# Kernel optimization log

Measured on AMD Instinct MI355X. Metric: run time of the kernel, lower is better.

Reference implementation:

```python
import jax, jax.numpy as jnp
import numpy as np

B, N, D = 256, 50, 128
NEG = -9e15  # torch uses -9000000000000000.0
LEAKY_SLOPE = 0.2


def setup_inputs() -> dict:
    key = jax.random.key(0)
    ks = jax.random.split(key, 6)
    hidden = jax.random.normal(ks[0], (B, N, D), dtype=jnp.float32)
    adj = jax.random.randint(ks[1], (B, N, N), 0, 5)  # edge types 0..4
    a_0 = jax.random.normal(ks[2], (D, 1), dtype=jnp.float32) * 0.05
    a_1 = jax.random.normal(ks[3], (D, 1), dtype=jnp.float32) * 0.05
    a_2 = jax.random.normal(ks[4], (D, 1), dtype=jnp.float32) * 0.05
    a_3 = jax.random.normal(ks[5], (D, 1), dtype=jnp.float32) * 0.05
    return {"hidden": hidden, "adj": adj, "a_0": a_0, "a_1": a_1, "a_2": a_2, "a_3": a_3}


def reference(hidden, adj, a_0, a_1, a_2, a_3):
    # LocalAggregator.forward (typed-edge GAT over session graph).
    # Original builds a_input[b,i,j,:] = h[b,i,:]*h[b,j,:] (B,N,N,D) then
    # projects with 4 relation vectors a_k (D,1). We fuse: stack the 4
    # vectors and contract D in one einsum -> e[b,k,i,j].
    A = jnp.concatenate([a_0, a_1, a_2, a_3], axis=1)          # (D, 4)
    e = jnp.einsum('bid,bjd,dk->bkij', hidden, hidden, A)      # (B, 4, N, N)
    e = jax.nn.leaky_relu(e, negative_slope=LEAKY_SLOPE)
    # Per-edge-type masking: adj value v in {1..4} selects branch v-1,
    # anything else gets -9e15 (same chained torch.where semantics/order).
    scores = jnp.full_like(e[:, 0], NEG)                        # (B, N, N)
    scores = jnp.where(adj == 1, e[:, 0], scores)
    scores = jnp.where(adj == 2, e[:, 1], scores)
    scores = jnp.where(adj == 3, e[:, 2], scores)
    scores = jnp.where(adj == 4, e[:, 3], scores)
    attn = jax.nn.softmax(scores, axis=-1)                      # (B, N, N)
    return jnp.einsum('bij,bjd->bid', attn, hidden)             # (B, N, D)
```

## Files before the change

kernel.cpp:

```cpp
#include <hip/hip_runtime.h>
#include <stdint.h>

typedef __attribute__((ext_vector_type(8))) short short8;
typedef __attribute__((ext_vector_type(4))) float f32x4;

namespace {
constexpr int   kN     = 50;
constexpr int   kD     = 128;
constexpr float kNeg   = -9.0e15f;
constexpr float kSlope = 0.2f;
constexpr int   HS32   = 132;
constexpr int   HS16   = 136;
constexpr int   ADS    = 52;
constexpr int   PS     = 20;
}

union Pack8 { uint32_t u[4]; short8 s; };

__global__ __launch_bounds__(512)
void gat_v11_kernel(const float* __restrict__ hidden,
                    const int*   __restrict__ adj,
                    const float* __restrict__ a0,
                    const float* __restrict__ a1,
                    const float* __restrict__ a2,
                    const float* __restrict__ a3,
                    float* __restrict__ out)
{
    __shared__ float          Hf [kN * HS32];
    __shared__ unsigned short Hhi[64 * HS16];
    __shared__ unsigned short Hlo[64 * HS16];
    __shared__ unsigned char  Ad [kN * ADS];
    __shared__ float          Xch[8][64][16];
    __shared__ unsigned short Pw [8][64 * PS];

    const int b    = blockIdx.x;
    const int tid  = threadIdx.x;
    const int lane = tid & 63;
    const int wid  = __builtin_amdgcn_readfirstlane(tid >> 6);
    const int g    = lane >> 4;
    const int f    = lane & 15;

    const float* __restrict__ hb   = hidden + (size_t)b * (kN * kD);
    const int*   __restrict__ adjb = adj    + (size_t)b * (kN * kN);
    float*       __restrict__ outb = out    + (size_t)b * (kN * kD);

    const float4* hg = reinterpret_cast<const float4*>(hb);
    #pragma unroll
    for (int it4 = 0; it4 < 4; ++it4) {
        const int idx = tid + it4 * 512;
        const int j   = idx >> 5;
        const int d4  = idx & 31;
        float4 v = make_float4(0.f, 0.f, 0.f, 0.f);
        if (j < kN) v = hg[j * 32 + d4];

        const uint32_t h0 = __float_as_uint(v.x) & 0xffff0000u;
        const uint32_t h1 = __float_as_uint(v.y) & 0xffff0000u;
        const uint32_t h2 = __float_as_uint(v.z) & 0xffff0000u;
        const uint32_t h3 = __float_as_uint(v.w) & 0xffff0000u;
        uint2 hiw;
        hiw.x = h1 | (h0 >> 16);
        hiw.y = h3 | (h2 >> 16);
        const float r0 = v.x - __uint_as_float(h0);
        const float r1 = v.y - __uint_as_float(h1);
        const float r2 = v.z - __uint_as_float(h2);
        const float r3 = v.w - __uint_as_float(h3);
        uint2 low;
        low.x = (__float_as_uint(r1) & 0xffff0000u) | (__float_as_uint(r0) >> 16);
        low.y = (__float_as_uint(r3) & 0xffff0000u) | (__float_as_uint(r2) >> 16);
        *reinterpret_cast<uint2*>(&Hhi[j * HS16 + 4 * d4]) = hiw;
        *reinterpret_cast<uint2*>(&Hlo[j * HS16 + 4 * d4]) = low;
        if (j < kN) *reinterpret_cast<float4*>(&Hf[j * HS32 + 4 * d4]) = v;
    }
    for (int idx = tid; idx < 625; idx += 512) {
        const int4 v = reinterpret_cast<const int4*>(adjb)[idx];
        const int e = 4 * idx;
        const int vv[4] = {v.x, v.y, v.z, v.w};
        #pragma unroll
        for (int p = 0; p < 4; ++p) {
            const int ee  = e + p;
            const int row = ee / kN;
            const int col = ee - kN * row;
            Ad[row * ADS + col] = (unsigned char)vv[p];
        }
    }
    __syncthreads();

    const int it   = wid & 3;
    const int kh   = wid >> 2;
    const int i0   = 16 * it;
    const int irow = (i0 + f < kN) ? (i0 + f) : (kN - 1);

    f32x4 acc[4][4];
    #pragma unroll
    for (int jt = 0; jt < 4; ++jt)
        #pragma unroll
        for (int k = 0; k < 4; ++k) acc[jt][k] = (f32x4){0.f, 0.f, 0.f, 0.f};

    const float* __restrict__ aks[4] = {a0, a1, a2, a3};

    #pragma unroll
    for (int ksl2 = 0; ksl2 < 2; ++ksl2) {
        const int dofs = 64 * kh + 32 * ksl2 + 8 * g;

        const float4 hA0 = *reinterpret_cast<const float4*>(&Hf[irow * HS32 + dofs]);
        const float4 hA1 = *reinterpret_cast<const float4*>(&Hf[irow * HS32 + dofs + 4]);
        const float ha[8] = {hA0.x, hA0.y, hA0.z, hA0.w, hA1.x, hA1.y, hA1.z, hA1.w};

        short8 qh[4], ql[4];
        #pragma unroll
        for (int k = 0; k < 4; ++k) {
            const float4 av0 = *reinterpret_cast<const float4*>(aks[k] + dofs);
            const float4 av1 = *reinterpret_cast<const float4*>(aks[k] + dofs + 4);
            const float aa[8] = {av0.x, av0.y, av0.z, av0.w, av1.x, av1.y, av1.z, av1.w};
            Pack8 ph, pl;
            #pragma unroll
            for (int p = 0; p < 4; ++p) {
                const float q0 = ha[2 * p]     * aa[2 * p];
                const float q1 = ha[2 * p + 1] * aa[2 * p + 1];
                const uint32_t b0 = __float_as_uint(q0) & 0xffff0000u;
                const uint32_t b1 = __float_as_uint(q1) & 0xffff0000u;
                ph.u[p] = b1 | (b0 >> 16);
                const float s0 = q0 - __uint_as_float(b0);
                const float s1 = q1 - __uint_as_float(b1);
                pl.u[p] = (__float_as_uint(s1) & 0xffff0000u) | (__float_as_uint(s0) >> 16);
            }
            qh[k] = ph.s;
            ql[k] = pl.s;
        }

        #pragma unroll
        for (int jt = 0; jt < 4; ++jt) {
            const int jrow = 16 * jt + f;
            const short8 bh = *reinterpret_cast<const short8*>(&Hhi[jrow * HS16 + dofs]);
            const short8 bl = *reinterpret_cast<const short8*>(&Hlo[jrow * HS16 + dofs]);
            #pragma unroll
            for (int k = 0; k < 4; ++k) {
                acc[jt][k] = __builtin_amdgcn_mfma_f32_16x16x32_bf16(qh[k], bh, acc[jt][k], 0, 0, 0);
                acc[jt][k] = __builtin_amdgcn_mfma_f32_16x16x32_bf16(qh[k], bl, acc[jt][k], 0, 0, 0);
                acc[jt][k] = __builtin_amdgcn_mfma_f32_16x16x32_bf16(ql[k], bh, acc[jt][k], 0, 0, 0);
            }
        }
    }

    f32x4 spart[4];
    uint32_t vmask = 0;
    #pragma unroll
    for (int jt = 0; jt < 4; ++jt) {
        const int j = 16 * jt + f;
        #pragma unroll
        for (int reg = 0; reg < 4; ++reg) {
            const int ii  = i0 + 4 * g + reg;
            const int iic = (ii < kN) ? ii : (kN - 1);
            int kv = 0;
            if (j < kN) kv = Ad[iic * ADS + j];
            const bool valid = (kv >= 1) && (kv <= 4);
            spart[jt][reg] = (kv == 1) ? acc[jt][0][reg]
                           : (kv == 2) ? acc[jt][1][reg]
                           : (kv == 3) ? acc[jt][2][reg]
                           : (kv == 4) ? acc[jt][3][reg] : 0.f;
            vmask |= (valid ? 1u : 0u) << (4 * jt + reg);
        }
    }

    #pragma unroll
    for (int jt = 0; jt < 4; ++jt)
        *reinterpret_cast<f32x4*>(&Xch[wid][lane][4 * jt]) = spart[jt];
    __syncthreads();

    float s[4][4];
    #pragma unroll
    for (int jt = 0; jt < 4; ++jt) {
        const f32x4 o = *reinterpret_cast<const f32x4*>(&Xch[wid ^ 4][lane][4 * jt]);
        #pragma unroll
        for (int reg = 0; reg < 4; ++reg) {
            const float x  = spart[jt][reg] + o[reg];
            const float lx = (x > 0.f) ? x : kSlope * x;
            s[jt][reg] = ((vmask >> (4 * jt + reg)) & 1u) ? lx : kNeg;
        }
    }

    #pragma unroll
    for (int reg = 0; reg < 4; ++reg) {
        float m = fmaxf(fmaxf(s[0][reg], s[1][reg]), fmaxf(s[2][reg], s[3][reg]));
        #pragma unroll
        for (int o = 1; o < 16; o <<= 1) m = fmaxf(m, __shfl_xor(m, o));

        float e[4];
        float t = 0.f;
        #pragma unroll
        for (int jt = 0; jt < 4; ++jt) {
            const int j = 16 * jt + f;
            e[jt] = (j < kN) ? __expf(s[jt][reg] - m) : 0.f;
            t += e[jt];
        }
        #pragma unroll
        for (int o = 1; o < 16; o <<= 1) t += __shfl_xor(t, o);

        const float inv = 1.0f / t;
        #pragma unroll
        for (int jt = 0; jt < 4; ++jt) {
            uint32_t u = __float_as_uint(e[jt] * inv);
            u += 0x7fffu + ((u >> 16) & 1u);
            Pw[wid][(16 * jt + f) * PS + 4 * g + reg] = (unsigned short)(u >> 16);
        }
    }

    {
        const int db = 64 * kh + 4 * f;
        f32x4 o0 = {0.f, 0.f, 0.f, 0.f}, o1 = o0, o2 = o0, o3 = o0;
        #pragma unroll 5
        for (int j = 0; j < kN; ++j) {
            const float4  hv = *reinterpret_cast<const float4*>(&Hf[j * HS32 + db]);
            const ushort4 p4 = *reinterpret_cast<const ushort4*>(&Pw[wid][j * PS + 4 * g]);
            const float av0 = __uint_as_float(((uint32_t)p4.x) << 16);
            const float av1 = __uint_as_float(((uint32_t)p4.y) << 16);
            const float av2 = __uint_as_float(((uint32_t)p4.z) << 16);
            const float av3 = __uint_as_float(((uint32_t)p4.w) << 16);
            o0.x += av0 * hv.x; o0.y += av0 * hv.y; o0.z += av0 * hv.z; o0.w += av0 * hv.w;
            o1.x += av1 * hv.x; o1.y += av1 * hv.y; o1.z += av1 * hv.z; o1.w += av1 * hv.w;
            o2.x += av2 * hv.x; o2.y += av2 * hv.y; o2.z += av2 * hv.z; o2.w += av2 * hv.w;
            o3.x += av3 * hv.x; o3.y += av3 * hv.y; o3.z += av3 * hv.z; o3.w += av3 * hv.w;
        }
        const int rbase = i0 + 4 * g;
        if (rbase + 0 < kN) *reinterpret_cast<f32x4*>(&outb[(rbase + 0) * kD + db]) = o0;
        if (rbase + 1 < kN) *reinterpret_cast<f32x4*>(&outb[(rbase + 1) * kD + db]) = o1;
        if (rbase + 2 < kN) *reinterpret_cast<f32x4*>(&outb[(rbase + 2) * kD + db]) = o2;
        if (rbase + 3 < kN) *reinterpret_cast<f32x4*>(&outb[(rbase + 3) * kD + db]) = o3;
    }
}

extern "C" void kernel_launch(void* const* d_in, const int* in_sizes, int n_in,
                              void* d_out, int out_size, void* d_ws, size_t ws_size,
                              hipStream_t stream) {
    const float* hidden = reinterpret_cast<const float*>(d_in[0]);
    const int*   adjp   = reinterpret_cast<const int*>(d_in[1]);
    const float* a0     = reinterpret_cast<const float*>(d_in[2]);
    const float* a1     = reinterpret_cast<const float*>(d_in[3]);
    const float* a2     = reinterpret_cast<const float*>(d_in[4]);
    const float* a3     = reinterpret_cast<const float*>(d_in[5]);
    float*       outp   = reinterpret_cast<float*>(d_out);

    gat_v11_kernel<<<dim3(256), dim3(512), 0, stream>>>(
        hidden, adjp, a0, a1, a2, a3, outp);
}
```

Baseline: 17.76 us.

## Compute attention-times-hidden with bf16 hi/lo MFMA using transposed split hidden

Replaces the scalar FMA loop for attn @ hidden with MFMA 16x16x32 bf16 instructions. Hidden is stored in a transposed, packed hi/lo bf16 layout so that two MFMAs (hi and lo parts) keep near-fp32 accuracy on the hidden operand. The fp32 hidden copy in shared memory is dropped, and the query row is rebuilt from the hi/lo halves. The price is an extra transposed staging pass at load time with strided LDS writes, plus unpacking work before each MFMA. Output stores become scalar rather than float4.

```diff
diff --git a/kernel.cpp b/kernel.cpp
--- a/kernel.cpp
+++ b/kernel.cpp
@@ -9,16 +9,23 @@
 constexpr int   kD     = 128;
 constexpr float kNeg   = -9.0e15f;
 constexpr float kSlope = 0.2f;
-constexpr int   HS32   = 132;
 constexpr int   HS16   = 136;
 constexpr int   ADS    = 52;
-constexpr int   PS     = 20;
+constexpr int   HTW    = 66;
+constexpr int   PW     = 72;
 }
 
 union Pack8 { uint32_t u[4]; short8 s; };
 
+__device__ __forceinline__ uint32_t pack_hl(float v) {
+    const uint32_t b  = __float_as_uint(v);
+    const uint32_t hi = b & 0xffff0000u;
+    const float    r  = v - __uint_as_float(hi);
+    return (b >> 16) | (__float_as_uint(r) & 0xffff0000u);
+}
+
 __global__ __launch_bounds__(512)
-void gat_v11_kernel(const float* __restrict__ hidden,
+void gat_v12_kernel(const float* __restrict__ hidden,
                     const int*   __restrict__ adj,
                     const float* __restrict__ a0,
                     const float* __restrict__ a1,
@@ -26,12 +33,12 @@
                     const float* __restrict__ a3,
                     float* __restrict__ out)
 {
-    __shared__ float          Hf [kN * HS32];
     __shared__ unsigned short Hhi[64 * HS16];
     __shared__ unsigned short Hlo[64 * HS16];
+    __shared__ uint32_t       Hti[128 * HTW];
     __shared__ unsigned char  Ad [kN * ADS];
     __shared__ float          Xch[8][64][16];
-    __shared__ unsigned short Pw [8][64 * PS];
+    __shared__ unsigned short Pw2[8][16 * PW];
 
     const int b    = blockIdx.x;
     const int tid  = threadIdx.x;
@@ -69,7 +76,6 @@
         low.y = (__float_as_uint(r3) & 0xffff0000u) | (__float_as_uint(r2) >> 16);
         *reinterpret_cast<uint2*>(&Hhi[j * HS16 + 4 * d4]) = hiw;
         *reinterpret_cast<uint2*>(&Hlo[j * HS16 + 4 * d4]) = low;
-        if (j < kN) *reinterpret_cast<float4*>(&Hf[j * HS32 + 4 * d4]) = v;
     }
     for (int idx = tid; idx < 625; idx += 512) {
         const int4 v = reinterpret_cast<const int4*>(adjb)[idx];
@@ -83,6 +89,21 @@
             Ad[row * ADS + col] = (unsigned char)vv[p];
         }
     }
+    const float2* hb2 = reinterpret_cast<const float2*>(hb);
+    #pragma unroll
+    for (int it4 = 0; it4 < 4; ++it4) {
+        const int jp = wid + 8 * it4;
+        const int j0 = 2 * jp, j1 = 2 * jp + 1;
+        const int d2 = lane;
+        float2 v0 = make_float2(0.f, 0.f), v1 = v0;
+        if (j0 < kN) v0 = hb2[j0 * 64 + d2];
+        if (j1 < kN) v1 = hb2[j1 * 64 + d2];
+        uint2 wa, wb;
+        wa.x = pack_hl(v0.x); wa.y = pack_hl(v1.x);
+        wb.x = pack_hl(v0.y); wb.y = pack_hl(v1.y);
+        *reinterpret_cast<uint2*>(&Hti[(2 * d2 + 0) * HTW + j0]) = wa;
+        *reinterpret_cast<uint2*>(&Hti[(2 * d2 + 1) * HTW + j0]) = wb;
+    }
     __syncthreads();
 
     const int it   = wid & 3;
@@ -102,9 +123,15 @@
     for (int ksl2 = 0; ksl2 < 2; ++ksl2) {
         const int dofs = 64 * kh + 32 * ksl2 + 8 * g;
 
-        const float4 hA0 = *reinterpret_cast<const float4*>(&Hf[irow * HS32 + dofs]);
-        const float4 hA1 = *reinterpret_cast<const float4*>(&Hf[irow * HS32 + dofs + 4]);
-        const float ha[8] = {hA0.x, hA0.y, hA0.z, hA0.w, hA1.x, hA1.y, hA1.z, hA1.w};
+        const short8 ah8 = *reinterpret_cast<const short8*>(&Hhi[irow * HS16 + dofs]);
+        const short8 al8 = *reinterpret_cast<const short8*>(&Hlo[irow * HS16 + dofs]);
+        float ha[8];
+        #pragma unroll
+        for (int p = 0; p < 8; ++p) {
+            const uint32_t uh = ((uint32_t)(unsigned short)ah8[p]) << 16;
+            const uint32_t ul = ((uint32_t)(unsigned short)al8[p]) << 16;
+            ha[p] = __uint_as_float(uh) + __uint_as_float(ul);
+        }
 
         short8 qh[4], ql[4];
         #pragma unroll
@@ -201,31 +228,54 @@
         for (int jt = 0; jt < 4; ++jt) {
             uint32_t u = __float_as_uint(e[jt] * inv);
             u += 0x7fffu + ((u >> 16) & 1u);
-            Pw[wid][(16 * jt + f) * PS + 4 * g + reg] = (unsigned short)(u >> 16);
+            Pw2[wid][(4 * g + reg) * PW + 16 * jt + f] = (unsigned short)(u >> 16);
         }
     }
 
     {
-        const int db = 64 * kh + 4 * f;
-        f32x4 o0 = {0.f, 0.f, 0.f, 0.f}, o1 = o0, o2 = o0, o3 = o0;
-        #pragma unroll 5
-        for (int j = 0; j < kN; ++j) {
-            const float4  hv = *reinterpret_cast<const float4*>(&Hf[j * HS32 + db]);
-            const ushort4 p4 = *reinterpret_cast<const ushort4*>(&Pw[wid][j * PS + 4 * g]);
-            const float av0 = __uint_as_float(((uint32_t)p4.x) << 16);
-            const float av1 = __uint_as_float(((uint32_t)p4.y) << 16);
-            const float av2 = __uint_as_float(((uint32_t)p4.z) << 16);
-            const float av3 = __uint_as_float(((uint32_t)p4.w) << 16);
-            o0.x += av0 * hv.x; o0.y += av0 * hv.y; o0.z += av0 * hv.z; o0.w += av0 * hv.w;
-            o1.x += av1 * hv.x; o1.y += av1 * hv.y; o1.z += av1 * hv.z; o1.w += av1 * hv.w;
-            o2.x += av2 * hv.x; o2.y += av2 * hv.y; o2.z += av2 * hv.z; o2.w += av2 * hv.w;
-            o3.x += av3 * hv.x; o3.y += av3 * hv.y; o3.z += av3 * hv.z; o3.w += av3 * hv.w;
-        }
-        const int rbase = i0 + 4 * g;
-        if (rbase + 0 < kN) *reinterpret_cast<f32x4*>(&outb[(rbase + 0) * kD + db]) = o0;
-        if (rbase + 1 < kN) *reinterpret_cast<f32x4*>(&outb[(rbase + 1) * kD + db]) = o1;
-        if (rbase + 2 < kN) *reinterpret_cast<f32x4*>(&outb[(rbase + 2) * kD + db]) = o2;
-        if (rbase + 3 < kN) *reinterpret_cast<f32x4*>(&outb[(rbase + 3) * kD + db]) = o3;
+        const int db = 64 * kh;
+
+        const short8 af0 = *reinterpret_cast<const short8*>(&Pw2[wid][f * PW + 0  + 8 * g]);
+        const short8 af1 = *reinterpret_cast<const short8*>(&Pw2[wid][f * PW + 32 + 8 * g]);
+
+        f32x4 acc2[4];
+        #pragma unroll
+        for (int dt = 0; dt < 4; ++dt) acc2[dt] = (f32x4){0.f, 0.f, 0.f, 0.f};
+
+        #pragma unroll
+        for (int dt = 0; dt < 4; ++dt) {
+            const int drow = db + 16 * dt + f;
+            #pragma unroll
+            for (int jc = 0; jc < 2; ++jc) {
+                const uint32_t* hp = &Hti[drow * HTW + 32 * jc + 8 * g];
+                const uint2 u01 = *reinterpret_cast<const uint2*>(hp + 0);
+                const uint2 u23 = *reinterpret_cast<const uint2*>(hp + 2);
+                const uint2 u45 = *reinterpret_cast<const uint2*>(hp + 4);
+                const uint2 u67 = *reinterpret_cast<const uint2*>(hp + 6);
+                Pack8 bh, bl;
+                bh.u[0] = (u01.x & 0xffffu) | (u01.y << 16);
+                bl.u[0] = (u01.x >> 16)     | (u01.y & 0xffff0000u);
+                bh.u[1] = (u23.x & 0xffffu) | (u23.y << 16);
+                bl.u[1] = (u23.x >> 16)     | (u23.y & 0xffff0000u);
+                bh.u[2] = (u45.x & 0xffffu) | (u45.y << 16);
+                bl.u[2] = (u45.x >> 16)     | (u45.y & 0xffff0000u);
+                bh.u[3] = (u67.x & 0xffffu) | (u67.y << 16);
+                bl.u[3] = (u67.x >> 16)     | (u67.y & 0xffff0000u);
+                const short8 a8 = jc ? af1 : af0;
+                acc2[dt] = __builtin_amdgcn_mfma_f32_16x16x32_bf16(a8, bh.s, acc2[dt], 0, 0, 0);
+                acc2[dt] = __builtin_amdgcn_mfma_f32_16x16x32_bf16(a8, bl.s, acc2[dt], 0, 0, 0);
+            }
+        }
+
+        #pragma unroll
+        for (int reg = 0; reg < 4; ++reg) {
+            const int ii = 16 * it + 4 * g + reg;
+            if (ii < kN) {
+                #pragma unroll
+                for (int dt = 0; dt < 4; ++dt)
+                    outb[ii * kD + db + 16 * dt + f] = acc2[dt][reg];
+            }
+        }
     }
 }
 
@@ -240,6 +290,6 @@
     const float* a3     = reinterpret_cast<const float*>(d_in[5]);
     float*       outp   = reinterpret_cast<float*>(d_out);
 
-    gat_v11_kernel<<<dim3(256), dim3(512), 0, stream>>>(
+    gat_v12_kernel<<<dim3(256), dim3(512), 0, stream>>>(
         hidden, adjp, a0, a1, a2, a3, outp);
 }
```

Result: faster. 16.98 us (-4.4%).
